# Kernel tuning notes

Measured on AMD Instinct MI355X. Metric: run time of the kernel, lower is better.

The kernel has to match this reference:

```python
import jax, jax.numpy as jnp
import numpy as np

# Llama-2-7B-like config with GQA
T, D, N, K, H = 2048, 4096, 32, 8, 128
THETA = 10000.0


def _rope(x, positions):
    """Split-ordering RoPE on last dim H of x: [..., T, heads, H]."""
    half = H // 2
    inv_freq = 1.0 / (THETA ** (jnp.arange(half, dtype=jnp.float32) / half))  # theta^(-2i/H)
    ang = positions.astype(jnp.float32)[:, None] * inv_freq[None, :]          # [T, half]
    cos = jnp.cos(ang)[:, None, :]
    sin = jnp.sin(ang)[:, None, :]
    x1, x2 = x[..., :half], x[..., half:]
    return jnp.concatenate([x1 * cos - x2 * sin, x2 * cos + x1 * sin], axis=-1).astype(x.dtype)


def setup_inputs() -> dict:
    key = jax.random.key(0)
    ks = jax.random.split(key, 5)
    s_in = 1.0 / np.sqrt(D)
    s_out = 1.0 / np.sqrt(N * H)
    return {
        "x": jax.random.normal(ks[0], (T, D), jnp.float32),
        "positions": jnp.arange(T, dtype=jnp.int32),
        "w_q": jax.random.normal(ks[1], (D, N, H), jnp.float32) * s_in,
        "w_k": jax.random.normal(ks[2], (D, K, H), jnp.float32) * s_in,
        "w_v": jax.random.normal(ks[3], (D, K, H), jnp.float32) * s_in,
        "w_o": jax.random.normal(ks[4], (N, H, D), jnp.float32) * s_out,
    }


def reference(x, positions, w_q, w_k, w_v, w_o):
    """Prefill path: fused QKV proj + RoPE + causal GQA attention + o_proj."""
    G = N // K  # query heads per kv head
    q = jnp.einsum('td,dnh->tnh', x, w_q)
    k = jnp.einsum('sd,dkh->skh', x, w_k)
    v = jnp.einsum('sd,dkh->skh', x, w_v)
    q = _rope(q, positions)
    k = _rope(k, positions)
    qg = q.reshape(T, K, G, H)
    scores = jnp.einsum('tkgh,skh->kgts', qg, k) * (H ** -0.5)
    causal = positions[:, None] >= positions[None, :]  # [T, S]
    scores = jnp.where(causal[None, None], scores, jnp.finfo(scores.dtype).min)
    probs = jax.nn.softmax(scores, axis=-1)
    out = jnp.einsum('kgts,skh->tkgh', probs, v).reshape(T, N, H)
    return jnp.einsum('tnh,nhd->td', out, w_o)
```

## Files before the change

### kernel.cpp

```cpp
#include <hip/hip_runtime.h>
#include <hip/hip_bf16.h>
#include <math.h>

#define T_SEQ   2048
#define D_MODEL 4096
#define N_Q     32
#define N_KV    8
#define HDIM    128
#define NH      (N_Q * HDIM)
#define KH      (N_KV * HDIM)
#define QKV_W   (NH + 2 * KH)

using bf16   = __hip_bfloat16;
using short8 = __attribute__((ext_vector_type(8))) short;
using floatx4 = __attribute__((ext_vector_type(4))) float;

__device__ __forceinline__ void load_lds16(const bf16* g, bf16* l) {
  __builtin_amdgcn_global_load_lds((const __attribute__((address_space(1))) void*)g,
                                   (__attribute__((address_space(3))) void*)l,
                                   16, 0, 0);
}

__global__ void cvt_bf16_kernel(const float* __restrict__ src, bf16* __restrict__ dst, int n4) {
  int i = blockIdx.x * 256 + threadIdx.x;
  if (i < n4) {
    const float4 v = ((const float4*)src)[i];
    union { bf16 h[4]; unsigned long long u; } o;
    o.h[0] = __float2bfloat16(v.x); o.h[1] = __float2bfloat16(v.y);
    o.h[2] = __float2bfloat16(v.z); o.h[3] = __float2bfloat16(v.w);
    ((unsigned long long*)dst)[i] = o.u;
  }
}

__global__ void sincos_tab(const int* __restrict__ pos, float* __restrict__ ct,
                           float* __restrict__ st) {
  const int i = blockIdx.x * 256 + threadIdx.x;
  const int t = i >> 6, h = i & 63;
  const float p = (float)pos[t];
  const float inv = exp2f(-(float)h * 0.20762050592420985f);
  float s, c; sincosf(p * inv, &s, &c);
  ct[i] = c; st[i] = s;
}

__global__ __launch_bounds__(256)
void transpose_cvt(const float* __restrict__ src, bf16* __restrict__ dst, int R, int C) {
  __shared__ float tile[64][65];
  const int bx = blockIdx.x * 64;
  const int by = blockIdx.y * 64;
  const int c4 = (threadIdx.x & 15) * 4;
  const int r0 = threadIdx.x >> 4;
#pragma unroll
  for (int i = 0; i < 4; i++) {
    const float4 v = *(const float4*)&src[(size_t)(by + r0 + i * 16) * C + bx + c4];
    tile[r0 + i * 16][c4 + 0] = v.x;
    tile[r0 + i * 16][c4 + 1] = v.y;
    tile[r0 + i * 16][c4 + 2] = v.z;
    tile[r0 + i * 16][c4 + 3] = v.w;
  }
  __syncthreads();
  const int cc = threadIdx.x >> 2;
  const int rq = (threadIdx.x & 3) * 16;
  union { bf16 h[8]; short8 s; } o0, o1;
#pragma unroll
  for (int j = 0; j < 8; j++) {
    o0.h[j] = __float2bfloat16(tile[rq + j][cc]);
    o1.h[j] = __float2bfloat16(tile[rq + 8 + j][cc]);
  }
  bf16* d = dst + (size_t)(bx + cc) * R + by + rq;
  *(short8*)(d)     = o0.s;
  *(short8*)(d + 8) = o1.s;
}

#define CS_STRIDE 137
template <int EPI>
__global__ __launch_bounds__(256)
void gemm_bt2(const bf16* __restrict__ A, const bf16* __restrict__ B,
              float* __restrict__ Cf, int N, int Kc, int hoff,
              const float* __restrict__ cosT, const float* __restrict__ sinT,
              bf16* __restrict__ Qo, bf16* __restrict__ Ko, bf16* __restrict__ Vo) {
  __shared__ bf16 smem[(EPI == 2) ? (128 * CS_STRIDE) : (128 * 128)];
  bf16* As = smem;
  bf16* Bs = smem + 128 * 64;

  const int tid  = threadIdx.x;
  const int lane = tid & 63;
  const int wave = tid >> 6;
  const int hy = blockIdx.y + hoff;
  const int bm = blockIdx.x * 128;
  const int bn = hy * 128;
  const int wm = (wave >> 1) * 64;
  const int wn = (wave & 1) * 64;
  const int r = lane & 15, q = lane >> 4;

  floatx4 acc[4][4];
  const floatx4 zero = {0.f, 0.f, 0.f, 0.f};
#pragma unroll
  for (int i = 0; i < 4; i++)
#pragma unroll
    for (int j = 0; j < 4; j++) acc[i][j] = zero;

  const int rl = lane >> 3, ch = lane & 7;
  const int srow = wave * 32 + rl;
  const int gch = ch ^ rl;
  const bf16* gA = A + (size_t)(bm + srow) * Kc + gch * 8;
  const bf16* gB = B + (size_t)(bn + srow) * Kc + gch * 8;

  for (int k0 = 0; k0 < Kc; k0 += 64) {
    __syncthreads();
#pragma unroll
    for (int i = 0; i < 4; i++)
      load_lds16(gA + k0 + (size_t)i * 8 * Kc, As + (wave * 32 + i * 8) * 64);
#pragma unroll
    for (int i = 0; i < 4; i++)
      load_lds16(gB + k0 + (size_t)i * 8 * Kc, Bs + (wave * 32 + i * 8) * 64);
    __syncthreads();

#pragma unroll
    for (int ks = 0; ks < 2; ks++) {
      short8 af[4], bfr[4];
#pragma unroll
      for (int mt = 0; mt < 4; mt++)
        af[mt] = *(const short8*)(As + (wm + mt * 16 + r) * 64 + ((ks * 4 + q) ^ (r & 7)) * 8);
#pragma unroll
      for (int nt = 0; nt < 4; nt++)
        bfr[nt] = *(const short8*)(Bs + (wn + nt * 16 + r) * 64 + ((ks * 4 + q) ^ (r & 7)) * 8);
#pragma unroll
      for (int mt = 0; mt < 4; mt++)
#pragma unroll
        for (int nt = 0; nt < 4; nt++)
          acc[mt][nt] = __builtin_amdgcn_mfma_f32_16x16x32_bf16(af[mt], bfr[nt], acc[mt][nt], 0, 0, 0);
    }
  }

  if (EPI == 1) {
#pragma unroll
    for (int mt = 0; mt < 4; mt++)
#pragma unroll
      for (int nt = 0; nt < 4; nt++)
#pragma unroll
        for (int reg = 0; reg < 4; reg++) {
          const int row = bm + wm + mt * 16 + q * 4 + reg;
          const int col = bn + wn + nt * 16 + r;
          Cf[(size_t)row * N + col] = acc[mt][nt][reg];
        }
  } else {
    __syncthreads();
#pragma unroll
    for (int mt = 0; mt < 4; mt++)
#pragma unroll
      for (int nt = 0; nt < 4; nt++)
#pragma unroll
        for (int reg = 0; reg < 4; reg++)
          smem[(wm + mt * 16 + q * 4 + reg) * CS_STRIDE + wn + nt * 16 + r] =
              __float2bfloat16(acc[mt][nt][reg]);
    __syncthreads();

    const int hn = hy;
    if (hn < N_Q + N_KV) {
      const float SCL = 0.12751744868673310f;
      const bool isQ = (hn < N_Q);
      bf16* base = isQ ? (Qo + (size_t)bm * NH + hn * HDIM)
                       : (Ko + (size_t)bm * KH + (hn - N_Q) * HDIM);
      const int ostride = isQ ? NH : KH;
      for (int idx = tid; idx < 128 * 64; idx += 256) {
        const int row = idx >> 6, h = idx & 63;
        const float x1 = __bfloat162float(smem[row * CS_STRIDE + h]);
        const float x2 = __bfloat162float(smem[row * CS_STRIDE + h + 64]);
        const float cs = cosT[(bm + row) * 64 + h];
        const float sn = sinT[(bm + row) * 64 + h];
        float o1 = x1 * cs - x2 * sn;
        float o2 = x2 * cs + x1 * sn;
        if (isQ) { o1 *= SCL; o2 *= SCL; }
        bf16* d = base + (size_t)row * ostride;
        d[h]      = __float2bfloat16(o1);
        d[h + 64] = __float2bfloat16(o2);
      }
    } else {
      const int kh = hn - (N_Q + N_KV);
      for (int idx = tid; idx < 128 * 32; idx += 256) {
        const int h = idx >> 5, r4 = (idx & 31) * 4;
        union { bf16 h4[4]; unsigned long long u; } o;
#pragma unroll
        for (int j = 0; j < 4; j++) o.h4[j] = smem[(r4 + j) * CS_STRIDE + h];
        *(unsigned long long*)(Vo + ((size_t)kh * HDIM + h) * T_SEQ + bm + r4) = o.u;
      }
    }
  }
}

#define MSHIFT 8.0f
__global__ __launch_bounds__(256, 2)
void flash_attn(const bf16* __restrict__ Q, const bf16* __restrict__ Kk,
                const bf16* __restrict__ Vt, bf16* __restrict__ O) {
  const int id = blockIdx.x;
  const int n  = id & 31;
  const int kh = n >> 2;
  const int bt = (id < 256) ? (15 - (id >> 5)) : ((id - 256) >> 5);
  const int t0 = bt * 128;
  const int tid = threadIdx.x, lane = tid & 63, w = tid >> 6;
  const int r = lane & 15, q = lane >> 4;

  __shared__ bf16 Ks[64][128];
  __shared__ bf16 Vs[128][64];
  __shared__ bf16 Ps[4][32][72];

  short8 qf[2][4];
#pragma unroll
  for (int mf = 0; mf < 2; mf++) {
    const bf16* qrow = Q + (size_t)(t0 + w * 32 + mf * 16 + r) * NH + n * HDIM;
#pragma unroll
    for (int ks = 0; ks < 4; ks++)
      qf[mf][ks] = *(const short8*)(qrow + ks * 32 + q * 8);
  }

  floatx4 o_acc[2][8];
  const floatx4 zero = {0.f, 0.f, 0.f, 0.f};
#pragma unroll
  for (int mf = 0; mf < 2; mf++)
#pragma unroll
    for (int i = 0; i < 8; i++) o_acc[mf][i] = zero;
  float l_lane[2][4];
#pragma unroll
  for (int mf = 0; mf < 2; mf++)
#pragma unroll
    for (int i = 0; i < 4; i++) l_lane[mf][i] = 0.f;

  const int krl = lane >> 4, kc = lane & 15;
  const int vrl = lane >> 3, vc = lane & 7;

  const int nIter = 2 * bt + 2;
  for (int it = 0; it < nIter; ++it) {
    const int s0 = it * 64;
    __syncthreads();
#pragma unroll
    for (int i = 0; i < 4; i++) {
      const int row = (w * 4 + i) * 4 + krl;
      load_lds16(Kk + (size_t)(s0 + row) * KH + kh * HDIM + (kc ^ (row & 7)) * 8,
                 &Ks[(w * 4 + i) * 4][0]);
    }
#pragma unroll
    for (int i = 0; i < 4; i++) {
      const int row = (w * 4 + i) * 8 + vrl;
      load_lds16(Vt + ((size_t)kh * HDIM + row) * T_SEQ + s0 + (vc ^ (row & 7)) * 8,
                 &Vs[(w * 4 + i) * 8][0]);
    }
    __syncthreads();

    floatx4 sa[2][4];
#pragma unroll
    for (int mf = 0; mf < 2; mf++)
#pragma unroll
      for (int nt = 0; nt < 4; nt++) sa[mf][nt] = zero;
#pragma unroll
    for (int ks = 0; ks < 4; ks++)
#pragma unroll
      for (int nt = 0; nt < 4; nt++) {
        const int krow = nt * 16 + r;
        const short8 kb = *(const short8*)(&Ks[krow][(((ks * 4 + q) ^ (krow & 7))) * 8]);
#pragma unroll
        for (int mf = 0; mf < 2; mf++)
          sa[mf][nt] = __builtin_amdgcn_mfma_f32_16x16x32_bf16(qf[mf][ks], kb, sa[mf][nt], 0, 0, 0);
      }

#pragma unroll
    for (int mf = 0; mf < 2; mf++) {
      const int rbase = t0 + w * 32 + mf * 16;
      if (s0 + 63 > rbase) {
#pragma unroll
        for (int nt = 0; nt < 4; nt++)
#pragma unroll
          for (int reg = 0; reg < 4; reg++) {
            const int trow = rbase + q * 4 + reg;
            const int scol = s0 + nt * 16 + r;
            if (scol > trow) sa[mf][nt][reg] = -INFINITY;
          }
      }
#pragma unroll
      for (int nt = 0; nt < 4; nt++)
#pragma unroll
        for (int reg = 0; reg < 4; reg++) {
          const float p = exp2f(sa[mf][nt][reg] - MSHIFT);
          l_lane[mf][reg] += p;
          Ps[w][mf * 16 + q * 4 + reg][nt * 16 + r] = __float2bfloat16(p);
        }
    }

    __asm__ volatile("s_waitcnt lgkmcnt(0)" ::: "memory");

#pragma unroll
    for (int ks = 0; ks < 2; ks++) {
      short8 pa[2];
#pragma unroll
      for (int mf = 0; mf < 2; mf++)
        pa[mf] = *(const short8*)(&Ps[w][mf * 16 + r][ks * 32 + q * 8]);
#pragma unroll
      for (int ht = 0; ht < 8; ht++) {
        const int vrow = ht * 16 + r;
        const short8 vb = *(const short8*)(&Vs[vrow][(((ks * 4 + q) ^ (vrow & 7))) * 8]);
#pragma unroll
        for (int mf = 0; mf < 2; mf++)
          o_acc[mf][ht] = __builtin_amdgcn_mfma_f32_16x16x32_bf16(pa[mf], vb, o_acc[mf][ht], 0, 0, 0);
      }
    }
  }

#pragma unroll
  for (int mf = 0; mf < 2; mf++)
#pragma unroll
    for (int reg = 0; reg < 4; reg++) {
      float v = l_lane[mf][reg];
      v += __shfl_xor(v, 1); v += __shfl_xor(v, 2);
      v += __shfl_xor(v, 4); v += __shfl_xor(v, 8);
      const float inv_l = 1.0f / v;
      const int trow = t0 + w * 32 + mf * 16 + q * 4 + reg;
#pragma unroll
      for (int ht = 0; ht < 8; ht++)
        O[(size_t)trow * NH + n * HDIM + ht * 16 + r] =
            __float2bfloat16(o_acc[mf][ht][reg] * inv_l);
    }
}

extern "C" void kernel_launch(void* const* d_in, const int* in_sizes, int n_in,
                              void* d_out, int out_size, void* d_ws, size_t ws_size,
                              hipStream_t stream) {
  (void)in_sizes; (void)n_in; (void)out_size; (void)ws_size;
  const float* x   = (const float*)d_in[0];
  const int* pos   = (const int*)d_in[1];
  const float* w_q = (const float*)d_in[2];
  const float* w_k = (const float*)d_in[3];
  const float* w_v = (const float*)d_in[4];
  const float* w_o = (const float*)d_in[5];
  float* out = (float*)d_out;

  char* ws = (char*)d_ws;
  bf16*  xb   = (bf16*)(ws);
  bf16*  Bq   = (bf16*)(ws + (16ULL << 20));
  bf16*  Qr   = (bf16*)(ws + (64ULL << 20));
  bf16*  Kr   = (bf16*)(ws + (80ULL << 20));
  bf16*  Vt   = (bf16*)(ws + (84ULL << 20));
  bf16*  Oatt = (bf16*)(ws + (88ULL << 20));
  float* ct   = (float*)(ws + (104ULL << 20));
  float* st   = (float*)(ws + (105ULL << 20));
  bf16*  woT  = Bq;

  cvt_bf16_kernel<<<(T_SEQ * D_MODEL / 4 + 255) / 256, 256, 0, stream>>>(x, xb, T_SEQ * D_MODEL / 4);
  sincos_tab<<<(T_SEQ * 64) / 256, 256, 0, stream>>>(pos, ct, st);
  transpose_cvt<<<dim3(NH / 64, D_MODEL / 64), 256, 0, stream>>>(w_q, Bq, D_MODEL, NH);
  transpose_cvt<<<dim3(KH / 64, D_MODEL / 64), 256, 0, stream>>>(w_k, Bq + (size_t)NH * D_MODEL, D_MODEL, KH);
  transpose_cvt<<<dim3(KH / 64, D_MODEL / 64), 256, 0, stream>>>(w_v, Bq + (size_t)(NH + KH) * D_MODEL, D_MODEL, KH);

  gemm_bt2<2><<<dim3(T_SEQ / 128, N_Q), 256, 0, stream>>>(
      xb, Bq, nullptr, QKV_W, D_MODEL, 0, ct, st, Qr, Kr, Vt);
  gemm_bt2<2><<<dim3(T_SEQ / 128, 2 * N_KV), 256, 0, stream>>>(
      xb, Bq, nullptr, QKV_W, D_MODEL, N_Q, ct, st, Qr, Kr, Vt);

  transpose_cvt<<<dim3(D_MODEL / 64, NH / 64), 256, 0, stream>>>(w_o, woT, NH, D_MODEL);

  flash_attn<<<dim3(512), 256, 0, stream>>>(Qr, Kr, Vt, Oatt);

  gemm_bt2<1><<<dim3(T_SEQ / 128, D_MODEL / 128), 256, 0, stream>>>(
      Oatt, woT, out, D_MODEL, NH, 0, nullptr, nullptr, nullptr, nullptr, nullptr);
}
```

Before: 540.7 us.

## Fuse prep kernels into one launch, merge QKV GEMMs, register-prefetch attention tiles

Combines the x conversion, sincos table and all weight transposes into one prep_all launch. When the workspace is large enough, w_o gets its own buffer so its transpose can run in that launch too. The Q and KV projection GEMMs become a single launch covering the full QKV width. Flash attention now prefetches the next K/V tile into registers and writes it to LDS, replacing async global-to-LDS loads. This cuts launch count and overlaps attention loads with compute, at the cost of more registers and a branchy prep kernel.

Result: faster. 495.9 us (-8.3%).

```diff
diff --git a/kernel.cpp b/kernel.cpp
--- a/kernel.cpp
+++ b/kernel.cpp
@@ -21,25 +21,68 @@
                                    16, 0, 0);
 }
 
-__global__ void cvt_bf16_kernel(const float* __restrict__ src, bf16* __restrict__ dst, int n4) {
-  int i = blockIdx.x * 256 + threadIdx.x;
-  if (i < n4) {
-    const float4 v = ((const float4*)src)[i];
+#define PB_CVT 8192
+#define PB_SIN 8704
+#define PB_WQ  12800
+#define PB_WK  13824
+#define PB_WV  14848
+#define PB_WO  18944
+__global__ __launch_bounds__(256)
+void prep_all(const float* __restrict__ x, const int* __restrict__ pos,
+              const float* __restrict__ w_q, const float* __restrict__ w_k,
+              const float* __restrict__ w_v, const float* __restrict__ w_o,
+              bf16* __restrict__ xb, float* __restrict__ ct, float* __restrict__ st,
+              bf16* __restrict__ Bq, bf16* __restrict__ woT) {
+  __shared__ float tile[64][65];
+  const int bid = blockIdx.x, tid = threadIdx.x;
+
+  if (bid < PB_CVT) {
+    const int i = bid * 256 + tid;
+    const float4 v = ((const float4*)x)[i];
     union { bf16 h[4]; unsigned long long u; } o;
     o.h[0] = __float2bfloat16(v.x); o.h[1] = __float2bfloat16(v.y);
     o.h[2] = __float2bfloat16(v.z); o.h[3] = __float2bfloat16(v.w);
-    ((unsigned long long*)dst)[i] = o.u;
-  }
-}
-
-__global__ void sincos_tab(const int* __restrict__ pos, float* __restrict__ ct,
-                           float* __restrict__ st) {
-  const int i = blockIdx.x * 256 + threadIdx.x;
-  const int t = i >> 6, h = i & 63;
-  const float p = (float)pos[t];
-  const float inv = exp2f(-(float)h * 0.20762050592420985f);
-  float s, c; sincosf(p * inv, &s, &c);
-  ct[i] = c; st[i] = s;
+    ((unsigned long long*)xb)[i] = o.u;
+    return;
+  }
+  if (bid < PB_SIN) {
+    const int i = (bid - PB_CVT) * 256 + tid;
+    const int t = i >> 6, h = i & 63;
+    const float p = (float)pos[t];
+    const float inv = exp2f(-(float)h * 0.20762050592420985f);
+    float s, c; sincosf(p * inv, &s, &c);
+    ct[i] = c; st[i] = s;
+    return;
+  }
+  const float* src; bf16* dst; int R, C, nx, local;
+  if (bid < PB_WQ)      { local = bid - PB_SIN; src = w_q; dst = Bq;                               R = D_MODEL; C = NH; nx = 64; }
+  else if (bid < PB_WK) { local = bid - PB_WQ;  src = w_k; dst = Bq + (size_t)NH * D_MODEL;        R = D_MODEL; C = KH; nx = 16; }
+  else if (bid < PB_WV) { local = bid - PB_WK;  src = w_v; dst = Bq + (size_t)(NH + KH) * D_MODEL; R = D_MODEL; C = KH; nx = 16; }
+  else                  { local = bid - PB_WV;  src = w_o; dst = woT;                              R = NH;      C = D_MODEL; nx = 64; }
+  const int bx = (local % nx) * 64;
+  const int by = (local / nx) * 64;
+  const int c4 = (tid & 15) * 4;
+  const int r0 = tid >> 4;
+#pragma unroll
+  for (int i = 0; i < 4; i++) {
+    const float4 v = *(const float4*)&src[(size_t)(by + r0 + i * 16) * C + bx + c4];
+    tile[r0 + i * 16][c4 + 0] = v.x;
+    tile[r0 + i * 16][c4 + 1] = v.y;
+    tile[r0 + i * 16][c4 + 2] = v.z;
+    tile[r0 + i * 16][c4 + 3] = v.w;
+  }
+  __syncthreads();
+  const int cc = tid >> 2;
+  const int rq = (tid & 3) * 16;
+  union { bf16 h[8]; short8 s; } o0, o1;
+#pragma unroll
+  for (int j = 0; j < 8; j++) {
+    o0.h[j] = __float2bfloat16(tile[rq + j][cc]);
+    o1.h[j] = __float2bfloat16(tile[rq + 8 + j][cc]);
+  }
+  bf16* d = dst + (size_t)(bx + cc) * R + by + rq;
+  *(short8*)(d)     = o0.s;
+  *(short8*)(d + 8) = o1.s;
 }
 
 __global__ __launch_bounds__(256)
@@ -228,23 +271,48 @@
   const int krl = lane >> 4, kc = lane & 15;
   const int vrl = lane >> 3, vc = lane & 7;
 
+  short8 kr[4], vr[4];
+#pragma unroll
+  for (int i = 0; i < 4; i++) {
+    const int row = (w * 4 + i) * 4 + krl;
+    kr[i] = *(const short8*)(Kk + (size_t)row * KH + kh * HDIM + (kc ^ (row & 7)) * 8);
+  }
+#pragma unroll
+  for (int i = 0; i < 4; i++) {
+    const int row = (w * 4 + i) * 8 + vrl;
+    vr[i] = *(const short8*)(Vt + ((size_t)(kh * HDIM + row)) * T_SEQ + (vc ^ (row & 7)) * 8);
+  }
+
   const int nIter = 2 * bt + 2;
   for (int it = 0; it < nIter; ++it) {
     const int s0 = it * 64;
     __syncthreads();
-#pragma unroll
-    for (int i = 0; i < 4; i++) {
-      const int row = (w * 4 + i) * 4 + krl;
-      load_lds16(Kk + (size_t)(s0 + row) * KH + kh * HDIM + (kc ^ (row & 7)) * 8,
-                 &Ks[(w * 4 + i) * 4][0]);
-    }
-#pragma unroll
-    for (int i = 0; i < 4; i++) {
-      const int row = (w * 4 + i) * 8 + vrl;
-      load_lds16(Vt + ((size_t)kh * HDIM + row) * T_SEQ + s0 + (vc ^ (row & 7)) * 8,
-                 &Vs[(w * 4 + i) * 8][0]);
-    }
-    __syncthreads();
+
+#pragma unroll
+    for (int i = 0; i < 4; i++)
+      *(short8*)(&Ks[(w * 4 + i) * 4][0] + lane * 8) = kr[i];
+#pragma unroll
+    for (int i = 0; i < 4; i++)
+      *(short8*)(&Vs[(w * 4 + i) * 8][0] + lane * 8) = vr[i];
+
+    if (it + 1 < nIter) {
+      const int s1 = s0 + 64;
+#pragma unroll
+      for (int i = 0; i < 4; i++) {
+        const int row = (w * 4 + i) * 4 + krl;
+        kr[i] = *(const short8*)(Kk + (size_t)(s1 + row) * KH + kh * HDIM + (kc ^ (row & 7)) * 8);
+      }
+#pragma unroll
+      for (int i = 0; i < 4; i++) {
+        const int row = (w * 4 + i) * 8 + vrl;
+        vr[i] = *(const short8*)(Vt + ((size_t)(kh * HDIM + row)) * T_SEQ + s1 + (vc ^ (row & 7)) * 8);
+      }
+    }
+
+    asm volatile("s_waitcnt lgkmcnt(0)" ::: "memory");
+    __builtin_amdgcn_sched_barrier(0);
+    __builtin_amdgcn_s_barrier();
+    __builtin_amdgcn_sched_barrier(0);
 
     floatx4 sa[2][4];
 #pragma unroll
@@ -323,7 +391,7 @@
 extern "C" void kernel_launch(void* const* d_in, const int* in_sizes, int n_in,
                               void* d_out, int out_size, void* d_ws, size_t ws_size,
                               hipStream_t stream) {
-  (void)in_sizes; (void)n_in; (void)out_size; (void)ws_size;
+  (void)in_sizes; (void)n_in; (void)out_size;
   const float* x   = (const float*)d_in[0];
   const int* pos   = (const int*)d_in[1];
   const float* w_q = (const float*)d_in[2];
@@ -341,20 +409,18 @@
   bf16*  Oatt = (bf16*)(ws + (88ULL << 20));
   float* ct   = (float*)(ws + (104ULL << 20));
   float* st   = (float*)(ws + (105ULL << 20));
-  bf16*  woT  = Bq;
-
-  cvt_bf16_kernel<<<(T_SEQ * D_MODEL / 4 + 255) / 256, 256, 0, stream>>>(x, xb, T_SEQ * D_MODEL / 4);
-  sincos_tab<<<(T_SEQ * 64) / 256, 256, 0, stream>>>(pos, ct, st);
-  transpose_cvt<<<dim3(NH / 64, D_MODEL / 64), 256, 0, stream>>>(w_q, Bq, D_MODEL, NH);
-  transpose_cvt<<<dim3(KH / 64, D_MODEL / 64), 256, 0, stream>>>(w_k, Bq + (size_t)NH * D_MODEL, D_MODEL, KH);
-  transpose_cvt<<<dim3(KH / 64, D_MODEL / 64), 256, 0, stream>>>(w_v, Bq + (size_t)(NH + KH) * D_MODEL, D_MODEL, KH);
-
-  gemm_bt2<2><<<dim3(T_SEQ / 128, N_Q), 256, 0, stream>>>(
+
+  const bool bigws = ws_size >= (138ULL << 20);
+  bf16* woT = bigws ? (bf16*)(ws + (106ULL << 20)) : Bq;
+
+  prep_all<<<bigws ? PB_WO : PB_WV, 256, 0, stream>>>(
+      x, pos, w_q, w_k, w_v, w_o, xb, ct, st, Bq, woT);
+
+  gemm_bt2<2><<<dim3(T_SEQ / 128, QKV_W / 128), 256, 0, stream>>>(
       xb, Bq, nullptr, QKV_W, D_MODEL, 0, ct, st, Qr, Kr, Vt);
-  gemm_bt2<2><<<dim3(T_SEQ / 128, 2 * N_KV), 256, 0, stream>>>(
-      xb, Bq, nullptr, QKV_W, D_MODEL, N_Q, ct, st, Qr, Kr, Vt);
-
-  transpose_cvt<<<dim3(D_MODEL / 64, NH / 64), 256, 0, stream>>>(w_o, woT, NH, D_MODEL);
+
+  if (!bigws)
+    transpose_cvt<<<dim3(D_MODEL / 64, NH / 64), 256, 0, stream>>>(w_o, woT, NH, D_MODEL);
 
   flash_attn<<<dim3(512), 256, 0, stream>>>(Qr, Kr, Vt, Oatt);
 
```
